# Kernel optimization log

Hardware: AMD Instinct MI355X
Metric: run time of the kernel (lower is better)

Reference implementation:

```python
import jax, jax.numpy as jnp
import numpy as np

B, T, DIM, H, KV, HD = 1, 2048, 2048, 16, 4, 128


def _rope_tables(T, hd):
    half = hd // 2
    inv_freq = 1.0 / (10000.0 ** (np.arange(0, half, dtype=np.float32) / half))
    t = np.arange(T, dtype=np.float32)
    freqs = np.outer(t, inv_freq)                # [T, hd/2]
    emb = np.concatenate([freqs, freqs], axis=-1)  # [T, hd]
    return jnp.asarray(np.cos(emb)), jnp.asarray(np.sin(emb))


def setup_inputs() -> dict:
    key = jax.random.key(0)
    kx, kq, kk, kv, ko = jax.random.split(key, 5)
    s = 0.02
    x = jax.random.normal(kx, (B, T, DIM), dtype=jnp.float32)
    wq = jax.random.normal(kq, (H * HD, DIM), dtype=jnp.float32) * s
    wk = jax.random.normal(kk, (KV * HD, DIM), dtype=jnp.float32) * s
    wv = jax.random.normal(kv, (KV * HD, DIM), dtype=jnp.float32) * s
    wo = jax.random.normal(ko, (DIM, H * HD), dtype=jnp.float32) * s
    cos, sin = _rope_tables(T, HD)
    return {"x": x, "wq": wq, "wk": wk, "wv": wv, "wo": wo, "cos": cos, "sin": sin}


def _rotate_half(u):
    u1, u2 = jnp.split(u, 2, axis=-1)
    return jnp.concatenate([-u2, u1], axis=-1)


def _apply_rope(u, cos, sin):
    # u: [B, T, h, hd]; cos/sin: [T, hd]
    c = cos[None, :, None, :]
    s = sin[None, :, None, :]
    return u * c + _rotate_half(u) * s


def reference(x, wq, wk, wv, wo, cos, sin):
    b, t, dim = x.shape
    hd = cos.shape[1]
    h = wq.shape[0] // hd
    kvh = wk.shape[0] // hd
    rep = h // kvh
    scale = hd ** -0.5

    q = (x @ wq.T).reshape(b, t, h, hd)
    k = (x @ wk.T).reshape(b, t, kvh, hd)
    v = (x @ wv.T).reshape(b, t, kvh, hd)

    q = _apply_rope(q, cos, sin)
    k = _apply_rope(k, cos, sin)

    # Group queries by shared KV head instead of materializing repeat_kv
    qg = q.reshape(b, t, kvh, rep, hd)
    scores = jnp.einsum('bqgrd,bkgd->bgrqk', qg, k) * scale  # [b,g,r,T,T]
    causal = jnp.tril(jnp.ones((t, t), dtype=bool))
    scores = jnp.where(causal[None, None, None], scores, jnp.float32(-1e30))
    attn = jax.nn.softmax(scores, axis=-1)
    out = jnp.einsum('bgrqk,bkgd->bqgrd', attn, v).reshape(b, t, h * hd)
    return out @ wo.T
```

## Files before the change

### kernel.cpp

```cpp
#include <hip/hip_runtime.h>
#include <hip/hip_bf16.h>

typedef unsigned short u16;
typedef __attribute__((ext_vector_type(8))) short bf16x8;
typedef __attribute__((ext_vector_type(8))) unsigned short u16x8;
typedef __attribute__((ext_vector_type(4))) float f32x4;

#define T_SEQ 2048
#define DIM   2048
#define NH    16
#define NKV   4
#define HD    128
#define NQKV  3072
#define SCALE 0.08838834764831845f
#define CHUNK 512

__device__ __forceinline__ u16 f2bf(float f) {
  unsigned int u = __float_as_uint(f);
  unsigned int r = (u + 0x7fffu + ((u >> 16) & 1u)) >> 16;
  return (u16)r;
}
__device__ __forceinline__ float bf2f(u16 v) {
  return __uint_as_float(((unsigned int)v) << 16);
}

#define B1 1048576
#define B2 2097152
#define B3 2359296
#define B4 2621440
#define B5 3670016
__global__ void cast_all(const float4* __restrict__ x,  const float4* __restrict__ wq,
                         const float4* __restrict__ wk, const float4* __restrict__ wv,
                         const float4* __restrict__ wo,
                         ushort4* __restrict__ xb, ushort4* __restrict__ wqkvb,
                         ushort4* __restrict__ wob) {
  int i = blockIdx.x * 256 + threadIdx.x;
  const float4* src; ushort4* dst; int j;
  if (i < B1)      { src = x;  dst = xb;               j = i; }
  else if (i < B2) { src = wq; dst = wqkvb;            j = i - B1; }
  else if (i < B3) { src = wk; dst = wqkvb + 1048576;  j = i - B2; }
  else if (i < B4) { src = wv; dst = wqkvb + 1310720;  j = i - B3; }
  else             { src = wo; dst = wob;              j = i - B4; }
  float4 v = src[j];
  ushort4 o;
  o.x = f2bf(v.x); o.y = f2bf(v.y); o.z = f2bf(v.z); o.w = f2bf(v.w);
  dst[j] = o;
}

#define BM 128
#define BN 64
#define BK 64
#define LDP 72

__global__ __launch_bounds__(256) void gemm_bt(
    const u16* __restrict__ A, const u16* __restrict__ W,
    float* __restrict__ Cf, u16* __restrict__ Cb, int M, int N, int K)
{
  __shared__ u16 As[BM * LDP];
  __shared__ u16 Bs[BN * LDP];
  const int tid  = threadIdx.x;
  const int lane = tid & 63;
  const int wave = tid >> 6;
  const int ln   = lane & 15;
  const int quad = lane >> 4;
  const int m0 = blockIdx.y * BM;
  const int n0 = blockIdx.x * BN;
  const int wm = wave * 32;

  const int sr = tid >> 3;
  const int sc = (tid & 7) * 8;

  f32x4 acc[2][4] = {};

  for (int k0 = 0; k0 < K; k0 += BK) {
#pragma unroll
    for (int c = 0; c < 4; ++c) {
      int row = c * 32 + sr;
      *(bf16x8*)&As[row * LDP + sc] =
          *(const bf16x8*)&A[(size_t)(m0 + row) * K + k0 + sc];
    }
#pragma unroll
    for (int c = 0; c < 2; ++c) {
      int row = c * 32 + sr;
      *(bf16x8*)&Bs[row * LDP + sc] =
          *(const bf16x8*)&W[(size_t)(n0 + row) * K + k0 + sc];
    }
    __syncthreads();
#pragma unroll
    for (int ks = 0; ks < 2; ++ks) {
      bf16x8 af[2], bfr[4];
#pragma unroll
      for (int mt = 0; mt < 2; ++mt)
        af[mt] = *(const bf16x8*)&As[(wm + mt * 16 + ln) * LDP + ks * 32 + quad * 8];
#pragma unroll
      for (int nt = 0; nt < 4; ++nt)
        bfr[nt] = *(const bf16x8*)&Bs[(nt * 16 + ln) * LDP + ks * 32 + quad * 8];
#pragma unroll
      for (int mt = 0; mt < 2; ++mt)
#pragma unroll
        for (int nt = 0; nt < 4; ++nt)
          acc[mt][nt] = __builtin_amdgcn_mfma_f32_16x16x32_bf16(
              af[mt], bfr[nt], acc[mt][nt], 0, 0, 0);
    }
    __syncthreads();
  }

#pragma unroll
  for (int mt = 0; mt < 2; ++mt)
#pragma unroll
    for (int nt = 0; nt < 4; ++nt)
#pragma unroll
      for (int r = 0; r < 4; ++r) {
        int row = m0 + wm + mt * 16 + quad * 4 + r;
        int col = n0 + nt * 16 + ln;
        if (Cb) Cb[(size_t)row * N + col] = f2bf(acc[mt][nt][r]);
        else    Cf[(size_t)row * N + col] = acc[mt][nt][r];
      }
}

__global__ __launch_bounds__(256) void gemm_qkv_sk(
    const u16* __restrict__ A, const u16* __restrict__ W,
    u16* __restrict__ Cp, int M, int N, int K)
{
  __shared__ u16 As[BM * LDP];
  __shared__ u16 Bs[BN * LDP];
  const int tid  = threadIdx.x;
  const int lane = tid & 63;
  const int wave = tid >> 6;
  const int ln   = lane & 15;
  const int quad = lane >> 4;
  const int m0 = blockIdx.y * BM;
  const int n0 = blockIdx.x * BN;
  const int wm = wave * 32;
  const int kBeg = blockIdx.z * (K >> 1);
  const int kEnd = kBeg + (K >> 1);
  u16* C = Cp + (size_t)blockIdx.z * M * N;

  const int sr = tid >> 3;
  const int sc = (tid & 7) * 8;

  f32x4 acc[2][4] = {};

  for (int k0 = kBeg; k0 < kEnd; k0 += BK) {
#pragma unroll
    for (int c = 0; c < 4; ++c) {
      int row = c * 32 + sr;
      *(bf16x8*)&As[row * LDP + sc] =
          *(const bf16x8*)&A[(size_t)(m0 + row) * K + k0 + sc];
    }
#pragma unroll
    for (int c = 0; c < 2; ++c) {
      int row = c * 32 + sr;
      *(bf16x8*)&Bs[row * LDP + sc] =
          *(const bf16x8*)&W[(size_t)(n0 + row) * K + k0 + sc];
    }
    __syncthreads();
#pragma unroll
    for (int ks = 0; ks < 2; ++ks) {
      bf16x8 af[2], bfr[4];
#pragma unroll
      for (int mt = 0; mt < 2; ++mt)
        af[mt] = *(const bf16x8*)&As[(wm + mt * 16 + ln) * LDP + ks * 32 + quad * 8];
#pragma unroll
      for (int nt = 0; nt < 4; ++nt)
        bfr[nt] = *(const bf16x8*)&Bs[(nt * 16 + ln) * LDP + ks * 32 + quad * 8];
#pragma unroll
      for (int mt = 0; mt < 2; ++mt)
#pragma unroll
        for (int nt = 0; nt < 4; ++nt)
          acc[mt][nt] = __builtin_amdgcn_mfma_f32_16x16x32_bf16(
              af[mt], bfr[nt], acc[mt][nt], 0, 0, 0);
    }
    __syncthreads();
  }

#pragma unroll
  for (int mt = 0; mt < 2; ++mt)
#pragma unroll
    for (int nt = 0; nt < 4; ++nt)
#pragma unroll
      for (int r = 0; r < 4; ++r) {
        int row = m0 + wm + mt * 16 + quad * 4 + r;
        int col = n0 + nt * 16 + ln;
        C[(size_t)row * N + col] = f2bf(acc[mt][nt][r]);
      }
}

__global__ __launch_bounds__(256) void rope_fused(
    const u16* __restrict__ P0, const u16* __restrict__ P1,
    const float* __restrict__ cosT, const float* __restrict__ sinT,
    u16* __restrict__ Qs, u16* __restrict__ Kb, u16* __restrict__ Vt)
{
  const int blk = blockIdx.x, tid = threadIdx.x;
  if (blk < 2048) {
    int e = blk * 2048 + tid * 8;
    int t = e >> 11, rem = e & 2047;
    int h = rem >> 7, d0 = rem & 127;
    size_t off = (size_t)t * NQKV + h * HD;
    u16x8 va = *(const u16x8*)&P0[off + d0];
    u16x8 vb = *(const u16x8*)&P1[off + d0];
    u16x8 pa = *(const u16x8*)&P0[off + (d0 ^ 64)];
    u16x8 pb = *(const u16x8*)&P1[off + (d0 ^ 64)];
    float4 c0 = *(const float4*)&cosT[t * HD + d0];
    float4 c1 = *(const float4*)&cosT[t * HD + d0 + 4];
    float4 s0 = *(const float4*)&sinT[t * HD + d0];
    float4 s1 = *(const float4*)&sinT[t * HD + d0 + 4];
    float cc[8] = {c0.x, c0.y, c0.z, c0.w, c1.x, c1.y, c1.z, c1.w};
    float ss[8] = {s0.x, s0.y, s0.z, s0.w, s1.x, s1.y, s1.z, s1.w};
    float sgn = (d0 < 64) ? -1.f : 1.f;
    u16x8 o;
#pragma unroll
    for (int j = 0; j < 8; ++j) {
      float u = bf2f(va[j]) + bf2f(vb[j]);
      float pr = bf2f(pa[j]) + bf2f(pb[j]);
      o[j] = f2bf((u * cc[j] + sgn * pr * ss[j]) * SCALE);
    }
    *(u16x8*)&Qs[(size_t)(t * NH + h) * HD + d0] = o;
  } else if (blk < 2560) {
    int e = (blk - 2048) * 2048 + tid * 8;
    int t = e >> 9, rem = e & 511;
    int g = rem >> 7, d0 = rem & 127;
    size_t off = (size_t)t * NQKV + DIM + g * HD;
    u16x8 va = *(const u16x8*)&P0[off + d0];
    u16x8 vb = *(const u16x8*)&P1[off + d0];
    u16x8 pa = *(const u16x8*)&P0[off + (d0 ^ 64)];
    u16x8 pb = *(const u16x8*)&P1[off + (d0 ^ 64)];
    float4 c0 = *(const float4*)&cosT[t * HD + d0];
    float4 c1 = *(const float4*)&cosT[t * HD + d0 + 4];
    float4 s0 = *(const float4*)&sinT[t * HD + d0];
    float4 s1 = *(const float4*)&sinT[t * HD + d0 + 4];
    float cc[8] = {c0.x, c0.y, c0.z, c0.w, c1.x, c1.y, c1.z, c1.w};
    float ss[8] = {s0.x, s0.y, s0.z, s0.w, s1.x, s1.y, s1.z, s1.w};
    float sgn = (d0 < 64) ? -1.f : 1.f;
    u16x8 o;
#pragma unroll
    for (int j = 0; j < 8; ++j) {
      float u = bf2f(va[j]) + bf2f(vb[j]);
      float pr = bf2f(pa[j]) + bf2f(pb[j]);
      o[j] = f2bf(u * cc[j] + sgn * pr * ss[j]);
    }
    *(u16x8*)&Kb[((size_t)g * T_SEQ + t) * HD + d0] = o;
  } else {
    __shared__ u16 Vls[64][72];
    int bv = blk - 2560;
    int g  = bv >> 6, rem = bv & 63;
    int dt = rem >> 5, tt = rem & 31;
    int t0 = tt * 64, db = dt * 64;
    {
      int lr = tid >> 2, lc = (tid & 3) * 16;
      size_t off = (size_t)(t0 + lr) * NQKV + DIM + NKV * HD + g * HD + db + lc;
      u16x8 a0 = *(const u16x8*)&P0[off],     b0 = *(const u16x8*)&P1[off];
      u16x8 a1 = *(const u16x8*)&P0[off + 8], b1 = *(const u16x8*)&P1[off + 8];
      u16x8 w0, w1;
#pragma unroll
      for (int j = 0; j < 8; ++j) {
        w0[j] = f2bf(bf2f(a0[j]) + bf2f(b0[j]));
        w1[j] = f2bf(bf2f(a1[j]) + bf2f(b1[j]));
      }
      *(u16x8*)&Vls[lr][lc]     = w0;
      *(u16x8*)&Vls[lr][lc + 8] = w1;
    }
    __syncthreads();
    {
      int dr = tid >> 2, tc = (tid & 3) * 16;
      u16x8 a, b;
#pragma unroll
      for (int j = 0; j < 8; ++j) {
        a[j] = Vls[tc + j][dr];
        b[j] = Vls[tc + 8 + j][dr];
      }
      u16* dst = Vt + (size_t)(g * HD + db + dr) * T_SEQ + t0 + tc;
      *(u16x8*)&dst[0] = a;
      *(u16x8*)&dst[8] = b;
    }
  }
}

#define KSP 136
#define VSP 72
#define PSP 72
__global__ __launch_bounds__(256) void flash_partial(
    const u16* __restrict__ Qs, const u16* __restrict__ Kb,
    const u16* __restrict__ Vt, u16* __restrict__ Opart,
    float* __restrict__ lpart)
{
  const int c  = blockIdx.x;
  const int qi = blockIdx.y;
  const int h  = blockIdx.z;
  const int b  = qi >> 2;
  if (c > b) return;
  const int g  = h >> 2;
  const int q0 = qi << 7;
  const int k0 = c << 9;
  const int kend = min(k0 + CHUNK, q0 + 128);

  __shared__ u16 Ks[64 * KSP];
  __shared__ u16 Vs[HD * VSP];
  __shared__ u16 Ps[4][32 * PSP];

  const int tid  = threadIdx.x;
  const int lane = tid & 63;
  const int w    = tid >> 6;
  const int ln   = lane & 15;
  const int quad = lane >> 4;

  bf16x8 aq[2][4];
#pragma unroll
  for (int mt = 0; mt < 2; ++mt) {
    const u16* qp = Qs + ((size_t)(q0 + w * 32 + mt * 16 + ln) * NH + h) * HD + quad * 8;
#pragma unroll
    for (int ks = 0; ks < 4; ++ks) aq[mt][ks] = *(const bf16x8*)&qp[ks * 32];
  }

  f32x4 o[2][8] = {};
  float rs[2][4] = {};

  const int rb0 = q0 + w * 32 + quad * 4;
  const int rb1 = rb0 + 16;
  const int rmax0 = q0 + w * 32 + 15;
  const int rmax1 = q0 + w * 32 + 31;

  const u16* kbase = Kb + (size_t)g * T_SEQ * HD;

  for (int jb = k0; jb < kend; jb += 64) {
    {
      int r = tid >> 4, cc = (tid & 15) * 8;
#pragma unroll
      for (int i = 0; i < 4; ++i) {
        int row = i * 16 + r;
        *(bf16x8*)&Ks[row * KSP + cc] =
            *(const bf16x8*)&kbase[(size_t)(jb + row) * HD + cc];
      }
    }
    {
      int r = tid >> 3, cc = (tid & 7) * 8;
#pragma unroll
      for (int i = 0; i < 4; ++i) {
        int row = i * 32 + r;
        *(bf16x8*)&Vs[row * VSP + cc] =
            *(const bf16x8*)&Vt[(size_t)(g * HD + row) * T_SEQ + jb + cc];
      }
    }
    __syncthreads();

    if (jb <= rmax1) {
      const bool do0  = (jb <= rmax0);
      const bool diag = (jb >= q0);

#pragma unroll
      for (int nb = 0; nb < 4; ++nb) {
        bf16x8 kf[4];
#pragma unroll
        for (int ks = 0; ks < 4; ++ks)
          kf[ks] = *(const bf16x8*)&Ks[(nb * 16 + ln) * KSP + ks * 32 + quad * 8];
        f32x4 s0 = {}, s1 = {};
#pragma unroll
        for (int ks = 0; ks < 4; ++ks) {
          if (do0) s0 = __builtin_amdgcn_mfma_f32_16x16x32_bf16(aq[0][ks], kf[ks], s0, 0, 0, 0);
          s1 = __builtin_amdgcn_mfma_f32_16x16x32_bf16(aq[1][ks], kf[ks], s1, 0, 0, 0);
        }
        const int j = jb + nb * 16 + ln;
#pragma unroll
        for (int r = 0; r < 4; ++r) {
          if (do0) {
            float p = (!diag || j <= rb0 + r) ? __expf(s0[r]) : 0.f;
            rs[0][r] += p;
            Ps[w][(quad * 4 + r) * PSP + nb * 16 + ln] = f2bf(p);
          }
          float p1 = (!diag || j <= rb1 + r) ? __expf(s1[r]) : 0.f;
          rs[1][r] += p1;
          Ps[w][(16 + quad * 4 + r) * PSP + nb * 16 + ln] = f2bf(p1);
        }
      }

#pragma unroll
      for (int kst = 0; kst < 2; ++kst) {
        bf16x8 ap0, ap1;
        if (do0) ap0 = *(const bf16x8*)&Ps[w][ln * PSP + kst * 32 + quad * 8];
        ap1 = *(const bf16x8*)&Ps[w][(16 + ln) * PSP + kst * 32 + quad * 8];
#pragma unroll
        for (int nb8 = 0; nb8 < 8; ++nb8) {
          bf16x8 bv = *(const bf16x8*)&Vs[(nb8 * 16 + ln) * VSP + kst * 32 + quad * 8];
          if (do0) o[0][nb8] = __builtin_amdgcn_mfma_f32_16x16x32_bf16(ap0, bv, o[0][nb8], 0, 0, 0);
          o[1][nb8] = __builtin_amdgcn_mfma_f32_16x16x32_bf16(ap1, bv, o[1][nb8], 0, 0, 0);
        }
      }
    }
    __syncthreads();
  }

  const int slot = h * 40 + 2 * b * (b + 1) + (qi & 3) * (b + 1) + c;
  u16*   op = Opart + (size_t)slot * (128 * 128);
  float* lp = lpart + (size_t)slot * 128;
#pragma unroll
  for (int mt = 0; mt < 2; ++mt) {
#pragma unroll
    for (int r = 0; r < 4; ++r)
#pragma unroll
      for (int off = 1; off < 16; off <<= 1)
        rs[mt][r] += __shfl_xor(rs[mt][r], off);
    int rowb = w * 32 + mt * 16 + quad * 4;
#pragma unroll
    for (int r = 0; r < 4; ++r) {
#pragma unroll
      for (int nb8 = 0; nb8 < 8; ++nb8)
        op[(rowb + r) * 128 + nb8 * 16 + ln] = f2bf(o[mt][nb8][r]);
      if (ln == 0) lp[rowb + r] = rs[mt][r];
    }
  }
}

__global__ __launch_bounds__(256) void flash_reduce(
    const u16* __restrict__ Opart, const float* __restrict__ lpart,
    u16* __restrict__ AO)
{
  const int h = blockIdx.y;
  const int tid = threadIdx.x;
  const int dgrp = tid & 15, trow = tid >> 4;
  const int t = blockIdx.x * 16 + trow;
  const int d0 = dgrp * 8;
  const int qi = t >> 7, r = t & 127;
  const int b = qi >> 2;
  const int base = h * 40 + 2 * b * (b + 1) + (qi & 3) * (b + 1);
  float so[8] = {};
  float sl = 0.f;
  for (int cc = 0; cc <= b; ++cc) {
    u16x8 ov = *(const u16x8*)&Opart[(size_t)(base + cc) * (128 * 128) + r * 128 + d0];
#pragma unroll
    for (int j = 0; j < 8; ++j) so[j] += bf2f(ov[j]);
    sl += lpart[(size_t)(base + cc) * 128 + r];
  }
  const float inv = 1.f / sl;
  u16x8 o;
#pragma unroll
  for (int j = 0; j < 8; ++j) o[j] = f2bf(so[j] * inv);
  *(u16x8*)&AO[(size_t)t * DIM + h * HD + d0] = o;
}

extern "C" void kernel_launch(void* const* d_in, const int* in_sizes, int n_in,
                              void* d_out, int out_size, void* d_ws, size_t ws_size,
                              hipStream_t stream) {
  const float* x    = (const float*)d_in[0];
  const float* wq   = (const float*)d_in[1];
  const float* wk   = (const float*)d_in[2];
  const float* wv   = (const float*)d_in[3];
  const float* wo   = (const float*)d_in[4];
  const float* cosT = (const float*)d_in[5];
  const float* sinT = (const float*)d_in[6];
  float* out = (float*)d_out;

  char* ws = (char*)d_ws;
  const size_t MB = 1024 * 1024;
  u16*   xb    = (u16*)(ws + 0 * MB);
  u16*   wqkvb = (u16*)(ws + 8 * MB);
  u16*   wob   = (u16*)(ws + 20 * MB);
  u16*   P0    = (u16*)(ws + 28 * MB);
  u16*   P1    = (u16*)(ws + 40 * MB);
  u16*   Qs    = (u16*)(ws + 8 * MB);
  u16*   Kb    = (u16*)(ws + 16 * MB);
  u16*   Vt    = (u16*)(ws + 18 * MB);
  u16*   AO    = (u16*)(ws + 0 * MB);
  u16*   Opart = (u16*)(ws + 28 * MB);
  float* lpart = (float*)(ws + 48 * MB);

  cast_all<<<B5 / 256, 256, 0, stream>>>(
      (const float4*)x, (const float4*)wq, (const float4*)wk, (const float4*)wv,
      (const float4*)wo, (ushort4*)xb, (ushort4*)wqkvb, (ushort4*)wob);

  gemm_qkv_sk<<<dim3(NQKV / BN, T_SEQ / BM, 2), 256, 0, stream>>>(
      xb, wqkvb, P0, T_SEQ, NQKV, DIM);

  rope_fused<<<2816, 256, 0, stream>>>(P0, P1, cosT, sinT, Qs, Kb, Vt);

  flash_partial<<<dim3(4, 16, 16), 256, 0, stream>>>(Qs, Kb, Vt, Opart, lpart);
  flash_reduce<<<dim3(T_SEQ / 16, NH), 256, 0, stream>>>(Opart, lpart, AO);

  gemm_bt<<<dim3(DIM / BN, T_SEQ / BM), 256, 0, stream>>>(
      AO, wob, out, nullptr, T_SEQ, DIM, DIM);
}
```

Baseline: 257.3 us.

## Keep attention probabilities in registers via transposed QK^T and lane shuffles

Computes S^T by swapping the MFMA operands, so each lane holds four consecutive key positions for one query row. The probabilities are packed to bf16 pairs and redistributed with cross-lane shuffles into the A-operand layout for the PV MFMA. This replaces the per-wave LDS P buffer and its store/load round trip, and simplifies the row-sum reduction. In exchange it adds shuffle instructions and register pressure, and its correctness depends on the exact MFMA lane layout.

```diff
diff --git a/kernel.cpp b/kernel.cpp
--- a/kernel.cpp
+++ b/kernel.cpp
@@ -22,6 +22,9 @@
 }
 __device__ __forceinline__ float bf2f(u16 v) {
   return __uint_as_float(((unsigned int)v) << 16);
+}
+__device__ __forceinline__ unsigned int packbf(float a, float b) {
+  return (unsigned int)f2bf(a) | ((unsigned int)f2bf(b) << 16);
 }
 
 #define B1 1048576
@@ -278,7 +281,6 @@
 
 #define KSP 136
 #define VSP 72
-#define PSP 72
 __global__ __launch_bounds__(256) void flash_partial(
     const u16* __restrict__ Qs, const u16* __restrict__ Kb,
     const u16* __restrict__ Vt, u16* __restrict__ Opart,
@@ -296,7 +298,6 @@
 
   __shared__ u16 Ks[64 * KSP];
   __shared__ u16 Vs[HD * VSP];
-  __shared__ u16 Ps[4][32 * PSP];
 
   const int tid  = threadIdx.x;
   const int lane = tid & 63;
@@ -313,14 +314,17 @@
   }
 
   f32x4 o[2][8] = {};
-  float rs[2][4] = {};
-
-  const int rb0 = q0 + w * 32 + quad * 4;
-  const int rb1 = rb0 + 16;
+  float rs0 = 0.f, rs1 = 0.f;
+
+  const int ql0 = q0 + w * 32 + ln;
+  const int ql1 = ql0 + 16;
   const int rmax0 = q0 + w * 32 + 15;
   const int rmax1 = q0 + w * 32 + 31;
 
   const u16* kbase = Kb + (size_t)g * T_SEQ * HD;
+
+  const int srcA = ln + ((quad & 1) * 2) * 16;
+  const int srcB = srcA + 16;
 
   for (int jb = k0; jb < kend; jb += 64) {
     {
@@ -347,6 +351,8 @@
       const bool do0  = (jb <= rmax0);
       const bool diag = (jb >= q0);
 
+      unsigned int w0_[4][2] = {}, w1_[4][2] = {};
+
 #pragma unroll
       for (int nb = 0; nb < 4; ++nb) {
         bf16x8 kf[4];
@@ -356,56 +362,78 @@
         f32x4 s0 = {}, s1 = {};
 #pragma unroll
         for (int ks = 0; ks < 4; ++ks) {
-          if (do0) s0 = __builtin_amdgcn_mfma_f32_16x16x32_bf16(aq[0][ks], kf[ks], s0, 0, 0, 0);
-          s1 = __builtin_amdgcn_mfma_f32_16x16x32_bf16(aq[1][ks], kf[ks], s1, 0, 0, 0);
+          if (do0) s0 = __builtin_amdgcn_mfma_f32_16x16x32_bf16(kf[ks], aq[0][ks], s0, 0, 0, 0);
+          s1 = __builtin_amdgcn_mfma_f32_16x16x32_bf16(kf[ks], aq[1][ks], s1, 0, 0, 0);
         }
-        const int j = jb + nb * 16 + ln;
+        const int j0 = jb + nb * 16 + quad * 4;
+        float p1[4];
 #pragma unroll
         for (int r = 0; r < 4; ++r) {
-          if (do0) {
-            float p = (!diag || j <= rb0 + r) ? __expf(s0[r]) : 0.f;
-            rs[0][r] += p;
-            Ps[w][(quad * 4 + r) * PSP + nb * 16 + ln] = f2bf(p);
+          p1[r] = (!diag || j0 + r <= ql1) ? __expf(s1[r]) : 0.f;
+          rs1 += p1[r];
+        }
+        w1_[nb][0] = packbf(p1[0], p1[1]);
+        w1_[nb][1] = packbf(p1[2], p1[3]);
+        if (do0) {
+          float p0[4];
+#pragma unroll
+          for (int r = 0; r < 4; ++r) {
+            p0[r] = (!diag || j0 + r <= ql0) ? __expf(s0[r]) : 0.f;
+            rs0 += p0[r];
           }
-          float p1 = (!diag || j <= rb1 + r) ? __expf(s1[r]) : 0.f;
-          rs[1][r] += p1;
-          Ps[w][(16 + quad * 4 + r) * PSP + nb * 16 + ln] = f2bf(p1);
+          w0_[nb][0] = packbf(p0[0], p0[1]);
+          w0_[nb][1] = packbf(p0[2], p0[3]);
         }
       }
 
 #pragma unroll
       for (int kst = 0; kst < 2; ++kst) {
-        bf16x8 ap0, ap1;
-        if (do0) ap0 = *(const bf16x8*)&Ps[w][ln * PSP + kst * 32 + quad * 8];
-        ap1 = *(const bf16x8*)&Ps[w][(16 + ln) * PSP + kst * 32 + quad * 8];
+        union { unsigned int u[4]; bf16x8 v; } a0c, a1c;
+#pragma unroll
+        for (int jw = 0; jw < 4; ++jw) {
+          const int src = (jw < 2) ? srcA : srcB;
+          unsigned int lo1 = (unsigned int)__shfl((int)w1_[2 * kst][jw & 1], src);
+          unsigned int hi1 = (unsigned int)__shfl((int)w1_[2 * kst + 1][jw & 1], src);
+          a1c.u[jw] = (quad < 2) ? lo1 : hi1;
+        }
+        if (do0) {
+#pragma unroll
+          for (int jw = 0; jw < 4; ++jw) {
+            const int src = (jw < 2) ? srcA : srcB;
+            unsigned int lo0 = (unsigned int)__shfl((int)w0_[2 * kst][jw & 1], src);
+            unsigned int hi0 = (unsigned int)__shfl((int)w0_[2 * kst + 1][jw & 1], src);
+            a0c.u[jw] = (quad < 2) ? lo0 : hi0;
+          }
+        }
 #pragma unroll
         for (int nb8 = 0; nb8 < 8; ++nb8) {
           bf16x8 bv = *(const bf16x8*)&Vs[(nb8 * 16 + ln) * VSP + kst * 32 + quad * 8];
-          if (do0) o[0][nb8] = __builtin_amdgcn_mfma_f32_16x16x32_bf16(ap0, bv, o[0][nb8], 0, 0, 0);
-          o[1][nb8] = __builtin_amdgcn_mfma_f32_16x16x32_bf16(ap1, bv, o[1][nb8], 0, 0, 0);
+          if (do0) o[0][nb8] = __builtin_amdgcn_mfma_f32_16x16x32_bf16(a0c.v, bv, o[0][nb8], 0, 0, 0);
+          o[1][nb8] = __builtin_amdgcn_mfma_f32_16x16x32_bf16(a1c.v, bv, o[1][nb8], 0, 0, 0);
         }
       }
     }
     __syncthreads();
   }
+
+  rs0 += __shfl_xor(rs0, 16); rs0 += __shfl_xor(rs0, 32);
+  rs1 += __shfl_xor(rs1, 16); rs1 += __shfl_xor(rs1, 32);
 
   const int slot = h * 40 + 2 * b * (b + 1) + (qi & 3) * (b + 1) + c;
   u16*   op = Opart + (size_t)slot * (128 * 128);
   float* lp = lpart + (size_t)slot * 128;
+  if (quad == 0) {
+    lp[w * 32 + ln]      = rs0;
+    lp[w * 32 + 16 + ln] = rs1;
+  }
 #pragma unroll
   for (int mt = 0; mt < 2; ++mt) {
-#pragma unroll
-    for (int r = 0; r < 4; ++r)
-#pragma unroll
-      for (int off = 1; off < 16; off <<= 1)
-        rs[mt][r] += __shfl_xor(rs[mt][r], off);
     int rowb = w * 32 + mt * 16 + quad * 4;
 #pragma unroll
     for (int r = 0; r < 4; ++r) {
 #pragma unroll
       for (int nb8 = 0; nb8 < 8; ++nb8)
         op[(rowb + r) * 128 + nb8 * 16 + ln] = f2bf(o[mt][nb8][r]);
-      if (ln == 0) lp[rowb + r] = rs[mt][r];
     }
   }
 }
```

Result: slower. 276.3 us (+7.4%).
